# Kernel tuning notes

Hardware: AMD Instinct MI355X
Metric: run time of the kernel (lower is better)

The kernel has to match this reference:

```python
import jax, jax.numpy as jnp
import numpy as np

D_MODEL = 1024
NUM_HEADS = 16
D_HEAD = 64
N_CTX = 2048
BATCH = 4
NEG_INF = -1e10  # matches torch masked_fill value


def setup_inputs() -> dict:
    key = jax.random.key(0)
    k1, k2, k3, k4, k5 = jax.random.split(key, 5)
    s = 1.0 / np.sqrt(D_MODEL).astype(np.float32)
    x = jax.random.normal(k1, (BATCH, N_CTX, D_MODEL), dtype=jnp.float32)
    W_K = jax.random.normal(k2, (NUM_HEADS, D_HEAD, D_MODEL), dtype=jnp.float32) * s
    W_Q = jax.random.normal(k3, (NUM_HEADS, D_HEAD, D_MODEL), dtype=jnp.float32) * s
    W_V = jax.random.normal(k4, (NUM_HEADS, D_HEAD, D_MODEL), dtype=jnp.float32) * s
    W_O = jax.random.normal(k5, (D_MODEL, NUM_HEADS * D_HEAD), dtype=jnp.float32) * s
    return {"x": x, "W_K": W_K, "W_Q": W_Q, "W_V": W_V, "W_O": W_O}


def reference(x, W_K, W_Q, W_V, W_O):
    b, q_len, d_model = x.shape
    d_head = W_K.shape[1]
    # projections: b=batch, p=pos, d=d_model, i=head, h=d_head
    K = jnp.einsum('bpd,ihd->biph', x, W_K)
    Q = jnp.einsum('bpd,ihd->biph', x, W_Q)
    V = jnp.einsum('bpd,ihd->biph', x, W_V)
    # scores[b, i, q, p] = Q[b,i,q,:] . K[b,i,p,:]
    scores = jnp.einsum('biph,biqh->biqp', K, Q)
    mask = jnp.tril(jnp.ones((q_len, q_len), dtype=bool))
    # NOTE: original masks with -1e10 BEFORE dividing by sqrt(d_head)
    scores = jnp.where(mask[None, None, :, :], scores, NEG_INF)
    attn = jax.nn.softmax(scores / np.sqrt(d_head).astype(np.float32), axis=-1)
    z = jnp.einsum('biph,biqp->biqh', V, attn)
    z_flat = jnp.transpose(z, (0, 2, 1, 3)).reshape(b, q_len, -1)  # b q (i h)
    out = jnp.einsum('bqf,df->bqd', z_flat, W_O)
    return out
```

## Files before the change

### kernel.cpp

```cpp
#include <hip/hip_runtime.h>
#include <hip/hip_bf16.h>


typedef short short8 __attribute__((ext_vector_type(8)));
typedef float f32x4 __attribute__((ext_vector_type(4)));

#define MFMA16(a, b, c) __builtin_amdgcn_mfma_f32_16x16x32_bf16((a), (b), (c), 0, 0, 0)

static __device__ __forceinline__ ushort f2bf(float f) {
  union { __hip_bfloat16 h; ushort u; } cv;
  cv.h = __float2bfloat16(f);
  return cv.u;
}

static __device__ __forceinline__ float fexp2(float x) {
#if __has_builtin(__builtin_amdgcn_exp2f)
  return __builtin_amdgcn_exp2f(x);
#else
  return __expf(x * 0.69314718056f);
#endif
}

static __device__ __forceinline__ void block_sync_lds() {
  asm volatile("s_waitcnt lgkmcnt(0)" ::: "memory");
  __builtin_amdgcn_s_barrier();
  __builtin_amdgcn_sched_barrier(0);
}

static __device__ __forceinline__ void block_sync_full() {
  asm volatile("s_waitcnt vmcnt(0) lgkmcnt(0)" ::: "memory");
  __builtin_amdgcn_s_barrier();
  __builtin_amdgcn_sched_barrier(0);
}

static __device__ __forceinline__ void store_out(float* p, float v) { *p = v; }
static __device__ __forceinline__ void store_out(__hip_bfloat16* p, float v) {
  *p = __float2bfloat16(v);
}

__global__ __launch_bounds__(256) void convert_all_kernel(
    const float* __restrict__ wq, const float* __restrict__ wk,
    const float* __restrict__ wv, const float* __restrict__ wo,
    const float* __restrict__ x, ushort* __restrict__ wqkv,
    ushort* __restrict__ wob, ushort* __restrict__ xb) {
  constexpr int W4 = 262144;
  constexpr size_t WSZ = (size_t)1024 * 1024;
  const int i = blockIdx.x * blockDim.x + threadIdx.x;
  const float* src;
  ushort* dst;
  int j;
  if (i < 2 * W4) {
    if (i < W4)      { src = wq; dst = wqkv;           j = i; }
    else             { src = wk; dst = wqkv + WSZ;     j = i - W4; }
  } else if (i < 4 * W4) {
    if (i < 3 * W4)  { src = wv; dst = wqkv + 2 * WSZ; j = i - 2 * W4; }
    else             { src = wo; dst = wob;            j = i - 3 * W4; }
  } else {
    src = x; dst = xb; j = i - 4 * W4;
  }
  const float4 v = ((const float4*)src)[j];
  ushort4 o;
  o.x = f2bf(v.x); o.y = f2bf(v.y); o.z = f2bf(v.z); o.w = f2bf(v.w);
  ((ushort4*)dst)[j] = o;
}

template <typename OUT_T>
__global__ __launch_bounds__(256, 2) void gemm_kernel(
    const ushort* __restrict__ A, int lda, const ushort* __restrict__ B, int ldb,
    OUT_T* __restrict__ C, int ldc, int K, int cpx) {
  __shared__ __align__(16) ushort As[2][128 * 64];
  __shared__ __align__(16) ushort Bs[2][128 * 64];
  const int tid = threadIdx.x;
  const int wave = tid >> 6, lane = tid & 63;
  const int lm = lane & 15, quad = lane >> 4;

  const int id = blockIdx.x;
  const int local = id >> 3;
  const int nt = (id & 7) * cpx + local % cpx;
  const int mt = local / cpx;
  const size_t m0 = (size_t)mt * 128;
  const size_t n0 = (size_t)nt * 128;

  const int rl = lane >> 3;
  const int cs = (lane & 7) ^ rl;
  const int fsw = lm & 7;
  const int wm = (wave >> 1) * 64, wn = (wave & 1) * 64;
  const int T = K >> 6;

#pragma unroll
  for (int j = 0; j < 4; ++j) {
    const int ch = wave * 4 + j;
    __builtin_amdgcn_global_load_lds(
        (const __attribute__((address_space(1))) void*)(B + (n0 + ch * 8 + rl) * (size_t)ldb + cs * 8),
        (__attribute__((address_space(3))) void*)(Bs[0] + ch * 512), 16, 0, 0);
    __builtin_amdgcn_global_load_lds(
        (const __attribute__((address_space(1))) void*)(A + (m0 + ch * 8 + rl) * (size_t)lda + cs * 8),
        (__attribute__((address_space(3))) void*)(As[0] + ch * 512), 16, 0, 0);
  }

  f32x4 acc[4][4] = {};
  for (int t = 0; t < T; ++t) {
    const int cur = t & 1;
    if (t + 1 < T) {
      const int k0 = (t + 1) << 6;
      ushort* an = As[cur ^ 1];
      ushort* bn = Bs[cur ^ 1];
#pragma unroll
      for (int j = 0; j < 4; ++j) {
        const int ch = wave * 4 + j;
        __builtin_amdgcn_global_load_lds(
            (const __attribute__((address_space(1))) void*)(B + (n0 + ch * 8 + rl) * (size_t)ldb + k0 + cs * 8),
            (__attribute__((address_space(3))) void*)(bn + ch * 512), 16, 0, 0);
        __builtin_amdgcn_global_load_lds(
            (const __attribute__((address_space(1))) void*)(A + (m0 + ch * 8 + rl) * (size_t)lda + k0 + cs * 8),
            (__attribute__((address_space(3))) void*)(an + ch * 512), 16, 0, 0);
      }
      asm volatile("s_waitcnt vmcnt(8)" ::: "memory");
    } else {
      asm volatile("s_waitcnt vmcnt(0)" ::: "memory");
    }
    __builtin_amdgcn_s_barrier();
    __builtin_amdgcn_sched_barrier(0);

    short8 a[4][2], b[4][2];
    const ushort* ab = As[cur];
    const ushort* bb = Bs[cur];
#pragma unroll
    for (int i = 0; i < 4; ++i) {
      const ushort* ar = ab + (wm + i * 16 + lm) * 64;
      const ushort* br = bb + (wn + i * 16 + lm) * 64;
#pragma unroll
      for (int ks = 0; ks < 2; ++ks) {
        const int off = (((ks * 4 + quad) ^ fsw) & 7) << 3;
        a[i][ks] = *(const short8*)(ar + off);
        b[i][ks] = *(const short8*)(br + off);
      }
    }
    asm volatile("s_waitcnt lgkmcnt(0)" ::: "memory");
    __builtin_amdgcn_s_barrier();
    __builtin_amdgcn_sched_barrier(0);

    __builtin_amdgcn_s_setprio(1);
#pragma unroll
    for (int i = 0; i < 4; ++i)
#pragma unroll
      for (int j = 0; j < 4; ++j)
#pragma unroll
        for (int ks = 0; ks < 2; ++ks)
          acc[i][j] = MFMA16(a[i][ks], b[j][ks], acc[i][j]);
    __builtin_amdgcn_s_setprio(0);
  }

  const int rq = quad * 4;
#pragma unroll
  for (int i = 0; i < 4; ++i)
#pragma unroll
    for (int j = 0; j < 4; ++j)
#pragma unroll
      for (int r = 0; r < 4; ++r)
        store_out(&C[(m0 + wm + i * 16 + rq + r) * (size_t)ldc + n0 + wn + j * 16 + lm],
                  acc[i][j][r]);
}

static __device__ __forceinline__ void vt_write8(ushort* vtbuf, int h0, int hsw,
                                                 int p, const short8& v) {
  const int pc = (p >> 3) ^ hsw;
  ushort* row = vtbuf + h0 * 64 + (p & 7);
#pragma unroll
  for (int u = 0; u < 8; ++u)
    row[u * 64 + (((pc ^ u) & 7) << 3)] = ((const ushort*)&v)[u];
}

static __device__ __forceinline__ void stage_k(const ushort* kglob, int pbase,
                                               ushort* kbuf, int wave, int lane) {
  const int rl = lane >> 3;
  const int c = (lane & 7) ^ rl;
#pragma unroll
  for (int j = 0; j < 2; ++j) {
    const int ch = wave * 2 + j;
    const ushort* src = kglob + (size_t)(pbase + ch * 8 + rl) * 3072 + c * 8;
    __builtin_amdgcn_global_load_lds(
        (const __attribute__((address_space(1))) void*)src,
        (__attribute__((address_space(3))) void*)(kbuf + ch * 512), 16, 0, 0);
  }
}

__global__ __launch_bounds__(256) void flash4_kernel(ushort* __restrict__ QKV) {
  constexpr int LD = 3072;
  __shared__ __align__(16) ushort vt[2][64 * 64];
  __shared__ __align__(16) ushort kt[2][64 * 64];
  __shared__ __align__(16) ushort pbuf[4][16 * 64];

  const int id = blockIdx.x;
  const int g = (id & 7) * 8 + ((id >> 3) & 7);
  const int m = id >> 6;
  const int head = g & 15;
  const int b = g >> 4;

  const int tid = threadIdx.x;
  const int wave = tid >> 6, lane = tid & 63;
  const int lm = lane & 15, quad = lane >> 4;

  const size_t qcol = (size_t)b * 2048 * LD + head * 64;
  const size_t vcol = qcol + 2048;
  const ushort* kglob = QKV + qcol + 1024;

  const int h0 = (tid & 7) * 8;
  const int hsw = tid & 7;
  const int plb = tid >> 3;
  const int psw = lm & 7;
  const int ksw = lm & 7;

  constexpr float CSC = 0.180336880f;
  const short8 vone = {0x3F80, 0x3F80, 0x3F80, 0x3F80,
                       0x3F80, 0x3F80, 0x3F80, 0x3F80};

  for (int pass = 0; pass < 2; ++pass) {
    const int qbi = pass ? 31 - m : m;
    const int qrow = qbi * 64 + wave * 16;
    const int qg = qrow + lm;
    const int nt = qbi + 1;

    const ushort* qp = QKV + qcol + (size_t)(qrow + lm) * LD;
    short8 qa0 = *(const short8*)(qp + quad * 8);
    short8 qa1 = *(const short8*)(qp + 32 + quad * 8);

    f32x4 accz[4] = {};
    f32x4 lacc = {};

    block_sync_lds();

    stage_k(kglob, 0, kt[0], wave, lane);
#pragma unroll
    for (int rr = 0; rr < 2; ++rr) {
      const int p = plb + rr * 32;
      short8 v = *(const short8*)(QKV + vcol + (size_t)p * LD + h0);
      vt_write8(vt[0], h0, hsw, p, v);
    }

    for (int it = 0; it < nt; ++it) {
      const int p0 = it * 64;
      block_sync_full();

      short8 ka[4], kb[4];
      const ushort* kbuf = kt[it & 1];
#pragma unroll
      for (int s = 0; s < 4; ++s) {
        const ushort* kr = kbuf + (s * 16 + lm) * 64;
        ka[s] = *(const short8*)(kr + (((quad ^ ksw) & 7) << 3));
        kb[s] = *(const short8*)(kr + ((((quad + 4) ^ ksw) & 7) << 3));
      }

      const bool more = (it + 1 < nt);
      short8 nv0, nv1;
      if (more) {
        nv0 = *(const short8*)(QKV + vcol + (size_t)(p0 + 64 + plb) * LD + h0);
        nv1 = *(const short8*)(QKV + vcol + (size_t)(p0 + 96 + plb) * LD + h0);
        stage_k(kglob, p0 + 64, kt[(it + 1) & 1], wave, lane);
      }

      f32x4 t4[4];
      __builtin_amdgcn_s_setprio(1);
#pragma unroll
      for (int s = 0; s < 4; ++s) {
        f32x4 t = {0.f, 0.f, 0.f, 0.f};
        t = MFMA16(ka[s], qa0, t);
        t = MFMA16(kb[s], qa1, t);
        t4[s] = t;
      }
      __builtin_amdgcn_s_setprio(0);

      float ps[4][4];
      if (it != nt - 1) {
#pragma unroll
        for (int s = 0; s < 4; ++s)
#pragma unroll
          for (int r = 0; r < 4; ++r)
            ps[s][r] = fexp2(t4[s][r] * CSC);
      } else {
#pragma unroll
        for (int s = 0; s < 4; ++s)
#pragma unroll
          for (int r = 0; r < 4; ++r) {
            const int pg = p0 + s * 16 + quad * 4 + r;
            const float e = fexp2(t4[s][r] * CSC);
            ps[s][r] = (pg > qg) ? 0.f : e;
          }
      }

      ushort* pw = pbuf[wave] + lm * 64;
#pragma unroll
      for (int s = 0; s < 4; ++s) {
        uint2 pk;
        pk.x = (uint)f2bf(ps[s][0]) | ((uint)f2bf(ps[s][1]) << 16);
        pk.y = (uint)f2bf(ps[s][2]) | ((uint)f2bf(ps[s][3]) << 16);
        *(uint2*)(pw + ((((2 * s + (quad >> 1)) ^ psw) & 7) << 3) +
                  ((quad & 1) << 2)) = pk;
      }

      const ushort* vbuf = vt[it & 1];
      __builtin_amdgcn_s_setprio(1);
#pragma unroll
      for (int kc = 0; kc < 2; ++kc) {
        short8 pa = *(const short8*)(pw + ((((kc * 4 + quad) ^ psw) & 7) << 3));
        lacc = MFMA16(pa, vone, lacc);
#pragma unroll
        for (int c = 0; c < 4; ++c) {
          const int hrow = c * 16 + lm;
          const int fh = ((hrow >> 3) ^ hrow) & 7;
          short8 vb = *(const short8*)(
              vbuf + hrow * 64 + ((((4 * kc + quad) ^ fh) & 7) << 3));
          accz[c] = MFMA16(pa, vb, accz[c]);
        }
      }
      __builtin_amdgcn_s_setprio(0);

      if (more) {
        ushort* nbuf = vt[(it + 1) & 1];
        vt_write8(nbuf, h0, hsw, plb, nv0);
        vt_write8(nbuf, h0, hsw, plb + 32, nv1);
      }
    }

#pragma unroll
    for (int r = 0; r < 4; ++r) {
      const float inv = 1.f / lacc[r];
#pragma unroll
      for (int c = 0; c < 4; ++c)
        QKV[qcol + (size_t)(qrow + quad * 4 + r) * LD + c * 16 + lm] =
            f2bf(accz[c][r] * inv);
    }
  }
}

extern "C" void kernel_launch(void* const* d_in, const int* in_sizes, int n_in,
                              void* d_out, int out_size, void* d_ws, size_t ws_size,
                              hipStream_t stream) {
  (void)in_sizes; (void)n_in; (void)out_size; (void)ws_size;
  const float* x  = (const float*)d_in[0];
  const float* wk = (const float*)d_in[1];
  const float* wq = (const float*)d_in[2];
  const float* wv = (const float*)d_in[3];
  const float* wo = (const float*)d_in[4];
  float* out = (float*)d_out;

  const size_t WSZ = (size_t)1024 * 1024;
  ushort* wqkv_b = (ushort*)d_ws;
  ushort* wo_b = wqkv_b + 3 * WSZ;
  ushort* QKV = wo_b + WSZ;
  ushort* xb = (ushort*)d_out;

  convert_all_kernel<<<12288, 256, 0, stream>>>(wq, wk, wv, wo, x,
                                                wqkv_b, wo_b, xb);

  gemm_kernel<__hip_bfloat16><<<1536, 256, 0, stream>>>(
      xb, 1024, wqkv_b, 1024, (__hip_bfloat16*)QKV, 3072, 1024, 3);

  flash4_kernel<<<1024, 256, 0, stream>>>(QKV);

  gemm_kernel<float><<<512, 256, 0, stream>>>(
      QKV, 3072, wo_b, 1024, out, 1024, 1024, 1);
}
```

Baseline: 253.3 us.

## Process two query blocks per workgroup to reuse staged K/V tiles

Each workgroup now handles a pair of adjacent 64-row query blocks (128 rows) per pass and shares every staged K and V tile between both, halving the grid from 1024 to 512 workgroups. The lower block skips the final diagonal tile. This roughly halves K/V global loads and LDS staging per query row. In exchange it adds register pressure from doubled accumulators and Q fragments, and halves the number of workgroups, which lowers occupancy and parallelism on the MI355X.

```diff
diff --git a/kernel.cpp b/kernel.cpp
--- a/kernel.cpp
+++ b/kernel.cpp
@@ -189,11 +189,11 @@
   constexpr int LD = 3072;
   __shared__ __align__(16) ushort vt[2][64 * 64];
   __shared__ __align__(16) ushort kt[2][64 * 64];
-  __shared__ __align__(16) ushort pbuf[4][16 * 64];
+  __shared__ __align__(16) ushort pbuf[4][2][16 * 64];
 
   const int id = blockIdx.x;
   const int g = (id & 7) * 8 + ((id >> 3) & 7);
-  const int m = id >> 6;
+  const int pairIdx = id >> 6;
   const int head = g & 15;
   const int b = g >> 4;
 
@@ -216,17 +216,22 @@
                        0x3F80, 0x3F80, 0x3F80, 0x3F80};
 
   for (int pass = 0; pass < 2; ++pass) {
-    const int qbi = pass ? 31 - m : m;
-    const int qrow = qbi * 64 + wave * 16;
-    const int qg = qrow + lm;
-    const int nt = qbi + 1;
-
-    const ushort* qp = QKV + qcol + (size_t)(qrow + lm) * LD;
-    short8 qa0 = *(const short8*)(qp + quad * 8);
-    short8 qa1 = *(const short8*)(qp + 32 + quad * 8);
-
-    f32x4 accz[4] = {};
-    f32x4 lacc = {};
+    const int QB = pass ? 15 - pairIdx : pairIdx;
+    const int np = 2 * QB + 2;
+    const int qrow0 = QB * 128 + wave * 16;
+    const int qrow1 = qrow0 + 64;
+    const int qg0 = qrow0 + lm;
+    const int qg1 = qrow1 + lm;
+
+    const ushort* qp0 = QKV + qcol + (size_t)(qrow0 + lm) * LD;
+    short8 qa00 = *(const short8*)(qp0 + quad * 8);
+    short8 qa01 = *(const short8*)(qp0 + 32 + quad * 8);
+    const ushort* qp1 = QKV + qcol + (size_t)(qrow1 + lm) * LD;
+    short8 qa10 = *(const short8*)(qp1 + quad * 8);
+    short8 qa11 = *(const short8*)(qp1 + 32 + quad * 8);
+
+    f32x4 accz0[4] = {}, accz1[4] = {};
+    f32x4 lacc0 = {}, lacc1 = {};
 
     block_sync_lds();
 
@@ -238,7 +243,7 @@
       vt_write8(vt[0], h0, hsw, p, v);
     }
 
-    for (int it = 0; it < nt; ++it) {
+    for (int it = 0; it < np; ++it) {
       const int p0 = it * 64;
       block_sync_full();
 
@@ -251,7 +256,7 @@
         kb[s] = *(const short8*)(kr + ((((quad + 4) ^ ksw) & 7) << 3));
       }
 
-      const bool more = (it + 1 < nt);
+      const bool more = (it + 1 < np);
       short8 nv0, nv1;
       if (more) {
         nv0 = *(const short8*)(QKV + vcol + (size_t)(p0 + 64 + plb) * LD + h0);
@@ -259,58 +264,105 @@
         stage_k(kglob, p0 + 64, kt[(it + 1) & 1], wave, lane);
       }
 
-      f32x4 t4[4];
+      const bool act0 = (it < np - 1);
+
+      f32x4 t40[4], t41[4];
       __builtin_amdgcn_s_setprio(1);
+      if (act0) {
+#pragma unroll
+        for (int s = 0; s < 4; ++s) {
+          f32x4 t = {0.f, 0.f, 0.f, 0.f};
+          t = MFMA16(ka[s], qa00, t);
+          t = MFMA16(kb[s], qa01, t);
+          t40[s] = t;
+        }
+      }
 #pragma unroll
       for (int s = 0; s < 4; ++s) {
         f32x4 t = {0.f, 0.f, 0.f, 0.f};
-        t = MFMA16(ka[s], qa0, t);
-        t = MFMA16(kb[s], qa1, t);
-        t4[s] = t;
+        t = MFMA16(ka[s], qa10, t);
+        t = MFMA16(kb[s], qa11, t);
+        t41[s] = t;
       }
       __builtin_amdgcn_s_setprio(0);
 
-      float ps[4][4];
-      if (it != nt - 1) {
-#pragma unroll
-        for (int s = 0; s < 4; ++s)
-#pragma unroll
-          for (int r = 0; r < 4; ++r)
-            ps[s][r] = fexp2(t4[s][r] * CSC);
-      } else {
-#pragma unroll
-        for (int s = 0; s < 4; ++s)
-#pragma unroll
-          for (int r = 0; r < 4; ++r) {
-            const int pg = p0 + s * 16 + quad * 4 + r;
-            const float e = fexp2(t4[s][r] * CSC);
-            ps[s][r] = (pg > qg) ? 0.f : e;
-          }
-      }
-
-      ushort* pw = pbuf[wave] + lm * 64;
-#pragma unroll
-      for (int s = 0; s < 4; ++s) {
-        uint2 pk;
-        pk.x = (uint)f2bf(ps[s][0]) | ((uint)f2bf(ps[s][1]) << 16);
-        pk.y = (uint)f2bf(ps[s][2]) | ((uint)f2bf(ps[s][3]) << 16);
-        *(uint2*)(pw + ((((2 * s + (quad >> 1)) ^ psw) & 7) << 3) +
-                  ((quad & 1) << 2)) = pk;
+      ushort* pw0 = &pbuf[wave][0][0] + lm * 64;
+      ushort* pw1 = &pbuf[wave][1][0] + lm * 64;
+
+      if (act0) {
+        float ps[4][4];
+        if (it != np - 2) {
+#pragma unroll
+          for (int s = 0; s < 4; ++s)
+#pragma unroll
+            for (int r = 0; r < 4; ++r)
+              ps[s][r] = fexp2(t40[s][r] * CSC);
+        } else {
+#pragma unroll
+          for (int s = 0; s < 4; ++s)
+#pragma unroll
+            for (int r = 0; r < 4; ++r) {
+              const int pg = p0 + s * 16 + quad * 4 + r;
+              const float e = fexp2(t40[s][r] * CSC);
+              ps[s][r] = (pg > qg0) ? 0.f : e;
+            }
+        }
+#pragma unroll
+        for (int s = 0; s < 4; ++s) {
+          uint2 pk;
+          pk.x = (uint)f2bf(ps[s][0]) | ((uint)f2bf(ps[s][1]) << 16);
+          pk.y = (uint)f2bf(ps[s][2]) | ((uint)f2bf(ps[s][3]) << 16);
+          *(uint2*)(pw0 + ((((2 * s + (quad >> 1)) ^ psw) & 7) << 3) +
+                    ((quad & 1) << 2)) = pk;
+        }
+      }
+
+      {
+        float ps[4][4];
+        if (it != np - 1) {
+#pragma unroll
+          for (int s = 0; s < 4; ++s)
+#pragma unroll
+            for (int r = 0; r < 4; ++r)
+              ps[s][r] = fexp2(t41[s][r] * CSC);
+        } else {
+#pragma unroll
+          for (int s = 0; s < 4; ++s)
+#pragma unroll
+            for (int r = 0; r < 4; ++r) {
+              const int pg = p0 + s * 16 + quad * 4 + r;
+              const float e = fexp2(t41[s][r] * CSC);
+              ps[s][r] = (pg > qg1) ? 0.f : e;
+            }
+        }
+#pragma unroll
+        for (int s = 0; s < 4; ++s) {
+          uint2 pk;
+          pk.x = (uint)f2bf(ps[s][0]) | ((uint)f2bf(ps[s][1]) << 16);
+          pk.y = (uint)f2bf(ps[s][2]) | ((uint)f2bf(ps[s][3]) << 16);
+          *(uint2*)(pw1 + ((((2 * s + (quad >> 1)) ^ psw) & 7) << 3) +
+                    ((quad & 1) << 2)) = pk;
+        }
       }
 
       const ushort* vbuf = vt[it & 1];
       __builtin_amdgcn_s_setprio(1);
 #pragma unroll
       for (int kc = 0; kc < 2; ++kc) {
-        short8 pa = *(const short8*)(pw + ((((kc * 4 + quad) ^ psw) & 7) << 3));
-        lacc = MFMA16(pa, vone, lacc);
+        const int poff = (((kc * 4 + quad) ^ psw) & 7) << 3;
+        short8 pa1v = *(const short8*)(pw1 + poff);
+        short8 pa0v;
+        if (act0) pa0v = *(const short8*)(pw0 + poff);
+        lacc1 = MFMA16(pa1v, vone, lacc1);
+        if (act0) lacc0 = MFMA16(pa0v, vone, lacc0);
 #pragma unroll
         for (int c = 0; c < 4; ++c) {
           const int hrow = c * 16 + lm;
           const int fh = ((hrow >> 3) ^ hrow) & 7;
           short8 vb = *(const short8*)(
               vbuf + hrow * 64 + ((((4 * kc + quad) ^ fh) & 7) << 3));
-          accz[c] = MFMA16(pa, vb, accz[c]);
+          accz1[c] = MFMA16(pa1v, vb, accz1[c]);
+          if (act0) accz0[c] = MFMA16(pa0v, vb, accz0[c]);
         }
       }
       __builtin_amdgcn_s_setprio(0);
@@ -324,11 +376,15 @@
 
 #pragma unroll
     for (int r = 0; r < 4; ++r) {
-      const float inv = 1.f / lacc[r];
-#pragma unroll
-      for (int c = 0; c < 4; ++c)
-        QKV[qcol + (size_t)(qrow + quad * 4 + r) * LD + c * 16 + lm] =
-            f2bf(accz[c][r] * inv);
+      const float inv0 = 1.f / lacc0[r];
+      const float inv1 = 1.f / lacc1[r];
+#pragma unroll
+      for (int c = 0; c < 4; ++c) {
+        QKV[qcol + (size_t)(qrow0 + quad * 4 + r) * LD + c * 16 + lm] =
+            f2bf(accz0[c][r] * inv0);
+        QKV[qcol + (size_t)(qrow1 + quad * 4 + r) * LD + c * 16 + lm] =
+            f2bf(accz1[c][r] * inv1);
+      }
     }
   }
 }
@@ -356,7 +412,7 @@
   gemm_kernel<__hip_bfloat16><<<1536, 256, 0, stream>>>(
       xb, 1024, wqkv_b, 1024, (__hip_bfloat16*)QKV, 3072, 1024, 3);
 
-  flash4_kernel<<<1024, 256, 0, stream>>>(QKV);
+  flash4_kernel<<<512, 256, 0, stream>>>(QKV);
 
   gemm_kernel<float><<<512, 256, 0, stream>>>(
       QKV, 3072, wo_b, 1024, out, 1024, 1024, 1);
```

New measurement: 302.7 us. 19.5% more time.
